# Kernel tuning notes

Measured on AMD Instinct MI355X. Metric: run time of the kernel, lower is better.

## Reference

```python
import jax, jax.numpy as jnp
import numpy as np

N_NODES = 50000


def _gcn_norm(edge_index, num_nodes):
    # PyG GCNConv default: add self-loops, symmetric normalization D^-1/2 A D^-1/2
    src, dst = edge_index[0], edge_index[1]
    loops = jnp.arange(num_nodes, dtype=src.dtype)
    src = jnp.concatenate([src, loops])
    dst = jnp.concatenate([dst, loops])
    deg = jax.ops.segment_sum(jnp.ones_like(src, dtype=jnp.float32), dst,
                              num_segments=num_nodes)
    dis = jnp.where(deg > 0, jax.lax.rsqrt(jnp.maximum(deg, 1.0)), 0.0)
    norm = dis[src] * dis[dst]  # [E']
    return src, dst, norm


def _gcn_conv(x, W, b, src, dst, norm, num_nodes):
    h = x @ W                                   # [N, out] transform first
    msg = h[src] * norm[:, None]                # [E', out] gather + scale
    agg = jax.ops.segment_sum(msg, dst, num_segments=num_nodes)  # scatter-add
    return agg + b


def setup_inputs() -> dict:
    key = jax.random.key(0)
    k1, k2, k3, k4 = jax.random.split(key, 4)
    n, e, d_in, d_h = N_NODES, 800000, 256, 128
    basic_block = jax.random.normal(k1, (n, d_in), dtype=jnp.float32)
    edge_index = jax.random.randint(k2, (2, e), 0, n, dtype=jnp.int64)
    W1 = jax.random.normal(k3, (d_in, d_h), dtype=jnp.float32) * (1.0 / np.sqrt(d_in))
    b1 = jnp.zeros((d_h,), dtype=jnp.float32)
    W2 = jax.random.normal(k4, (d_h, d_h), dtype=jnp.float32) * (1.0 / np.sqrt(d_h))
    b2 = jnp.zeros((d_h,), dtype=jnp.float32)
    return {"basic_block": basic_block, "edge_index": edge_index,
            "W1": W1, "b1": b1, "W2": W2, "b2": b2}


def reference(basic_block, edge_index, W1, b1, W2, b2):
    n = basic_block.shape[0]
    src, dst, norm = _gcn_norm(edge_index, n)
    x = jax.nn.relu(_gcn_conv(basic_block, W1, b1, src, dst, norm, n))
    x = _gcn_conv(x, W2, b2, src, dst, norm, n)
    return x
```

## Files before the change

kernel.cpp:

```cpp
#include <hip/hip_runtime.h>
#include <hip/hip_bf16.h>
#include <stdint.h>

#define D_H 128

typedef __bf16 bf16_t;
typedef unsigned short u16;
typedef bf16_t bf16x8 __attribute__((ext_vector_type(8)));
typedef bf16_t bf16x4 __attribute__((ext_vector_type(4)));
typedef float  f32x4  __attribute__((ext_vector_type(4)));

__global__ void k_countrank(const int* __restrict__ dst, int* __restrict__ cnt,
                            u16* __restrict__ rank, int E) {
    int e = blockIdx.x * 256 + threadIdx.x;
    if (e < E) rank[e] = (u16)atomicAdd(&cnt[dst[e]], 1);
}

__global__ __launch_bounds__(1024) void k_scan1(const int* __restrict__ cnt,
                                                int* __restrict__ out,
                                                int* __restrict__ bsums,
                                                float* __restrict__ dis, int N) {
    __shared__ int tmp[1024];
    int t = threadIdx.x;
    int i = blockIdx.x * 1024 + t;
    int v = (i < N) ? cnt[i] : 0;
    if (i < N) dis[i] = 1.0f / sqrtf((float)(v + 1));
    tmp[t] = v;
    __syncthreads();
    for (int d = 1; d < 1024; d <<= 1) {
        int x = (t >= d) ? tmp[t - d] : 0;
        __syncthreads();
        tmp[t] += x;
        __syncthreads();
    }
    if (i < N) out[i] = tmp[t] - v;
    if (t == 1023) bsums[blockIdx.x] = tmp[t];
}

__global__ void k_scan2(int* __restrict__ bsums, int nb) {
    __shared__ int tmp[64];
    int t = threadIdx.x;
    int v = (t < nb) ? bsums[t] : 0;
    tmp[t] = v;
    __syncthreads();
    for (int d = 1; d < 64; d <<= 1) {
        int x = (t >= d) ? tmp[t - d] : 0;
        __syncthreads();
        tmp[t] += x;
        __syncthreads();
    }
    if (t < nb) bsums[t] = tmp[t] - v;
}

__global__ __launch_bounds__(1024) void k_scan3(int* __restrict__ off,
                                                const int* __restrict__ bsums,
                                                int N, int E) {
    int i = blockIdx.x * 1024 + threadIdx.x;
    if (i < N) off[i] += bsums[blockIdx.x];
    if (i == 0) off[N] = E;
}

__global__ void k_prepw(const float* __restrict__ W, bf16_t* __restrict__ Wh,
                        bf16_t* __restrict__ Wl, int K) {
    int id = blockIdx.x * 256 + threadIdx.x;
    if (id >= K * 128) return;
    int k = id >> 7;
    int n = id & 127;
    float w = W[id];
    bf16_t h = (bf16_t)w;
    bf16_t l = (bf16_t)(w - (float)h);
    Wh[(size_t)n * K + k] = h;
    Wl[(size_t)n * K + k] = l;
}

#define LDK 40
__global__ __launch_bounds__(128) void k_mm1fill(
        const float* __restrict__ Af,
        const bf16_t* __restrict__ Wh, const bf16_t* __restrict__ Wl,
        const float* __restrict__ dis, bf16_t* __restrict__ Cb,
        int N, int K, int mmBlocks,
        const int* __restrict__ src, const int* __restrict__ dst,
        const int* __restrict__ off, const u16* __restrict__ rank,
        u16* __restrict__ csr16, int E) {
    __shared__ bf16_t AsH[64][LDK];
    __shared__ bf16_t AsL[64][LDK];
    __shared__ bf16_t BsH[128][LDK];
    __shared__ bf16_t BsL[128][LDK];

    if ((int)blockIdx.x >= mmBlocks) {
        int e = ((int)blockIdx.x - mmBlocks) * 128 + threadIdx.x;
        if (e < E) {
            int d = dst[e];
            csr16[off[d] + (int)rank[e]] = (u16)src[e];
        }
        return;
    }

    const int t    = threadIdx.x;
    const int lane = t & 63;
    const int wave = t >> 6;
    const int row0 = blockIdx.x * 64;
    const int wn   = wave * 64;
    const int fm   = lane & 15;
    const int fq   = lane >> 4;

    f32x4 acc[4][4] = {};

    for (int k0 = 0; k0 < K; k0 += 32) {
        __syncthreads();
#pragma unroll
        for (int i = 0; i < 4; i++) {
            int idx = t + i * 128;
            int r   = idx >> 3;
            int c4  = idx & 7;
            int gr  = row0 + r;
            float4 v = make_float4(0.f, 0.f, 0.f, 0.f);
            if (gr < N) v = *(const float4*)(Af + (size_t)gr * K + k0 + c4 * 4);
            bf16_t h0 = (bf16_t)v.x, h1 = (bf16_t)v.y, h2 = (bf16_t)v.z, h3 = (bf16_t)v.w;
            bf16_t l0 = (bf16_t)(v.x - (float)h0);
            bf16_t l1 = (bf16_t)(v.y - (float)h1);
            bf16_t l2 = (bf16_t)(v.z - (float)h2);
            bf16_t l3 = (bf16_t)(v.w - (float)h3);
            *(bf16x4*)&AsH[r][c4 * 4] = (bf16x4){h0, h1, h2, h3};
            *(bf16x4*)&AsL[r][c4 * 4] = (bf16x4){l0, l1, l2, l3};
        }
#pragma unroll
        for (int i = 0; i < 4; i++) {
            int idx = t + i * 128;
            int r   = idx >> 2;
            int c8  = idx & 3;
            *(bf16x8*)&BsH[r][c8 * 8] = *(const bf16x8*)(Wh + (size_t)r * K + k0 + c8 * 8);
            *(bf16x8*)&BsL[r][c8 * 8] = *(const bf16x8*)(Wl + (size_t)r * K + k0 + c8 * 8);
        }
        __syncthreads();

        bf16x8 ah[4], al[4], bh[4], bl[4];
#pragma unroll
        for (int i = 0; i < 4; i++) {
            ah[i] = *(const bf16x8*)&AsH[i * 16 + fm][fq * 8];
            al[i] = *(const bf16x8*)&AsL[i * 16 + fm][fq * 8];
            bh[i] = *(const bf16x8*)&BsH[wn + i * 16 + fm][fq * 8];
            bl[i] = *(const bf16x8*)&BsL[wn + i * 16 + fm][fq * 8];
        }
#pragma unroll
        for (int mi = 0; mi < 4; mi++)
#pragma unroll
            for (int ni = 0; ni < 4; ni++) {
                acc[mi][ni] = __builtin_amdgcn_mfma_f32_16x16x32_bf16(ah[mi], bh[ni], acc[mi][ni], 0, 0, 0);
                acc[mi][ni] = __builtin_amdgcn_mfma_f32_16x16x32_bf16(ah[mi], bl[ni], acc[mi][ni], 0, 0, 0);
                acc[mi][ni] = __builtin_amdgcn_mfma_f32_16x16x32_bf16(al[mi], bh[ni], acc[mi][ni], 0, 0, 0);
            }
    }

#pragma unroll
    for (int mi = 0; mi < 4; mi++)
#pragma unroll
        for (int r = 0; r < 4; r++) {
            int grow = row0 + mi * 16 + fq * 4 + r;
            if (grow < N) {
                float dr = dis[grow];
#pragma unroll
                for (int ni = 0; ni < 4; ni++)
                    Cb[(size_t)grow * D_H + wn + ni * 16 + fm] = (bf16_t)(dr * acc[mi][ni][r]);
            }
        }
}

__global__ __launch_bounds__(128) void k_mm2(const bf16_t* __restrict__ Ah,
                                             const bf16_t* __restrict__ Al,
                                             const bf16_t* __restrict__ Wh,
                                             const bf16_t* __restrict__ Wl,
                                             const float* __restrict__ dis,
                                             bf16_t* __restrict__ Cb,
                                             int N, int K) {
    __shared__ bf16_t AsH[64][LDK];
    __shared__ bf16_t AsL[64][LDK];
    __shared__ bf16_t BsH[128][LDK];
    __shared__ bf16_t BsL[128][LDK];

    const int t    = threadIdx.x;
    const int lane = t & 63;
    const int wave = t >> 6;
    const int row0 = blockIdx.x * 64;
    const int wn   = wave * 64;
    const int fm   = lane & 15;
    const int fq   = lane >> 4;

    f32x4 acc[4][4] = {};

    for (int k0 = 0; k0 < K; k0 += 32) {
        __syncthreads();
#pragma unroll
        for (int i = 0; i < 2; i++) {
            int idx = t + i * 128;
            int r   = idx >> 2;
            int c8  = idx & 3;
            int gr  = row0 + r;
            bf16x8 vh = {}, vl = {};
            if (gr < N) {
                vh = *(const bf16x8*)(Ah + (size_t)gr * K + k0 + c8 * 8);
                vl = *(const bf16x8*)(Al + (size_t)gr * K + k0 + c8 * 8);
            }
            *(bf16x8*)&AsH[r][c8 * 8] = vh;
            *(bf16x8*)&AsL[r][c8 * 8] = vl;
        }
#pragma unroll
        for (int i = 0; i < 4; i++) {
            int idx = t + i * 128;
            int r   = idx >> 2;
            int c8  = idx & 3;
            *(bf16x8*)&BsH[r][c8 * 8] = *(const bf16x8*)(Wh + (size_t)r * K + k0 + c8 * 8);
            *(bf16x8*)&BsL[r][c8 * 8] = *(const bf16x8*)(Wl + (size_t)r * K + k0 + c8 * 8);
        }
        __syncthreads();

        bf16x8 ah[4], al[4], bh[4], bl[4];
#pragma unroll
        for (int i = 0; i < 4; i++) {
            ah[i] = *(const bf16x8*)&AsH[i * 16 + fm][fq * 8];
            al[i] = *(const bf16x8*)&AsL[i * 16 + fm][fq * 8];
            bh[i] = *(const bf16x8*)&BsH[wn + i * 16 + fm][fq * 8];
            bl[i] = *(const bf16x8*)&BsL[wn + i * 16 + fm][fq * 8];
        }
#pragma unroll
        for (int mi = 0; mi < 4; mi++)
#pragma unroll
            for (int ni = 0; ni < 4; ni++) {
                acc[mi][ni] = __builtin_amdgcn_mfma_f32_16x16x32_bf16(ah[mi], bh[ni], acc[mi][ni], 0, 0, 0);
                acc[mi][ni] = __builtin_amdgcn_mfma_f32_16x16x32_bf16(ah[mi], bl[ni], acc[mi][ni], 0, 0, 0);
                acc[mi][ni] = __builtin_amdgcn_mfma_f32_16x16x32_bf16(al[mi], bh[ni], acc[mi][ni], 0, 0, 0);
            }
    }

#pragma unroll
    for (int mi = 0; mi < 4; mi++)
#pragma unroll
        for (int r = 0; r < 4; r++) {
            int grow = row0 + mi * 16 + fq * 4 + r;
            if (grow < N) {
                float dr = dis[grow];
#pragma unroll
                for (int ni = 0; ni < 4; ni++)
                    Cb[(size_t)grow * D_H + wn + ni * 16 + fm] = (bf16_t)(dr * acc[mi][ni][r]);
            }
        }
}

__global__ __launch_bounds__(256) void k_agg(const bf16_t* __restrict__ Hb,
                                             const float* __restrict__ dis,
                                             const int* __restrict__ off,
                                             const u16* __restrict__ csr16,
                                             const float4* __restrict__ bias4,
                                             float4* __restrict__ outF,
                                             bf16_t* __restrict__ outH,
                                             bf16_t* __restrict__ outL,
                                             int N, int mode) {
    const int half = threadIdx.x >> 5;
    const int lane = threadIdx.x & 31;
    const int node = blockIdx.x * 8 + half;
    if (node >= N) return;

    const size_t loff = (size_t)lane * 4;

    bf16x4 vs = *(const bf16x4*)(Hb + (size_t)node * D_H + loff);
    float4 a0 = make_float4((float)vs[0], (float)vs[1], (float)vs[2], (float)vs[3]);
    float4 a1 = {0,0,0,0}, a2 = {0,0,0,0}, a3 = {0,0,0,0};
    float4 a4 = {0,0,0,0}, a5 = {0,0,0,0}, a6 = {0,0,0,0}, a7 = {0,0,0,0};

    int p  = off[node];
    int p1 = off[node + 1];

    for (; p + 8 <= p1; p += 8) {
        int s0 = (int)csr16[p + 0], s1 = (int)csr16[p + 1];
        int s2 = (int)csr16[p + 2], s3 = (int)csr16[p + 3];
        int s4 = (int)csr16[p + 4], s5 = (int)csr16[p + 5];
        int s6 = (int)csr16[p + 6], s7 = (int)csr16[p + 7];
        bf16x4 h0 = *(const bf16x4*)(Hb + (size_t)s0 * D_H + loff);
        bf16x4 h1 = *(const bf16x4*)(Hb + (size_t)s1 * D_H + loff);
        bf16x4 h2 = *(const bf16x4*)(Hb + (size_t)s2 * D_H + loff);
        bf16x4 h3 = *(const bf16x4*)(Hb + (size_t)s3 * D_H + loff);
        bf16x4 h4 = *(const bf16x4*)(Hb + (size_t)s4 * D_H + loff);
        bf16x4 h5 = *(const bf16x4*)(Hb + (size_t)s5 * D_H + loff);
        bf16x4 h6 = *(const bf16x4*)(Hb + (size_t)s6 * D_H + loff);
        bf16x4 h7 = *(const bf16x4*)(Hb + (size_t)s7 * D_H + loff);
        a0.x += (float)h0[0]; a0.y += (float)h0[1]; a0.z += (float)h0[2]; a0.w += (float)h0[3];
        a1.x += (float)h1[0]; a1.y += (float)h1[1]; a1.z += (float)h1[2]; a1.w += (float)h1[3];
        a2.x += (float)h2[0]; a2.y += (float)h2[1]; a2.z += (float)h2[2]; a2.w += (float)h2[3];
        a3.x += (float)h3[0]; a3.y += (float)h3[1]; a3.z += (float)h3[2]; a3.w += (float)h3[3];
        a4.x += (float)h4[0]; a4.y += (float)h4[1]; a4.z += (float)h4[2]; a4.w += (float)h4[3];
        a5.x += (float)h5[0]; a5.y += (float)h5[1]; a5.z += (float)h5[2]; a5.w += (float)h5[3];
        a6.x += (float)h6[0]; a6.y += (float)h6[1]; a6.z += (float)h6[2]; a6.w += (float)h6[3];
        a7.x += (float)h7[0]; a7.y += (float)h7[1]; a7.z += (float)h7[2]; a7.w += (float)h7[3];
    }
    if (p + 4 <= p1) {
        int s0 = (int)csr16[p + 0], s1 = (int)csr16[p + 1];
        int s2 = (int)csr16[p + 2], s3 = (int)csr16[p + 3];
        bf16x4 h0 = *(const bf16x4*)(Hb + (size_t)s0 * D_H + loff);
        bf16x4 h1 = *(const bf16x4*)(Hb + (size_t)s1 * D_H + loff);
        bf16x4 h2 = *(const bf16x4*)(Hb + (size_t)s2 * D_H + loff);
        bf16x4 h3 = *(const bf16x4*)(Hb + (size_t)s3 * D_H + loff);
        a0.x += (float)h0[0]; a0.y += (float)h0[1]; a0.z += (float)h0[2]; a0.w += (float)h0[3];
        a1.x += (float)h1[0]; a1.y += (float)h1[1]; a1.z += (float)h1[2]; a1.w += (float)h1[3];
        a2.x += (float)h2[0]; a2.y += (float)h2[1]; a2.z += (float)h2[2]; a2.w += (float)h2[3];
        a3.x += (float)h3[0]; a3.y += (float)h3[1]; a3.z += (float)h3[2]; a3.w += (float)h3[3];
        p += 4;
    }
    for (; p < p1; p++) {
        int s0 = (int)csr16[p];
        bf16x4 h0 = *(const bf16x4*)(Hb + (size_t)s0 * D_H + loff);
        a0.x += (float)h0[0]; a0.y += (float)h0[1]; a0.z += (float)h0[2]; a0.w += (float)h0[3];
    }

    float4 sum;
    sum.x = ((a0.x + a1.x) + (a2.x + a3.x)) + ((a4.x + a5.x) + (a6.x + a7.x));
    sum.y = ((a0.y + a1.y) + (a2.y + a3.y)) + ((a4.y + a5.y) + (a6.y + a7.y));
    sum.z = ((a0.z + a1.z) + (a2.z + a3.z)) + ((a4.z + a5.z) + (a6.z + a7.z));
    sum.w = ((a0.w + a1.w) + (a2.w + a3.w)) + ((a4.w + a5.w) + (a6.w + a7.w));

    const float  di = dis[node];
    const float4 bv = bias4[lane];
    float vx = fmaf(di, sum.x, bv.x);
    float vy = fmaf(di, sum.y, bv.y);
    float vz = fmaf(di, sum.z, bv.z);
    float vw = fmaf(di, sum.w, bv.w);

    if (mode == 1) {
        vx = fmaxf(vx, 0.0f); vy = fmaxf(vy, 0.0f);
        vz = fmaxf(vz, 0.0f); vw = fmaxf(vw, 0.0f);
        bf16_t hx = (bf16_t)vx, hy = (bf16_t)vy, hz = (bf16_t)vz, hw = (bf16_t)vw;
        bf16_t lx = (bf16_t)(vx - (float)hx);
        bf16_t ly = (bf16_t)(vy - (float)hy);
        bf16_t lz = (bf16_t)(vz - (float)hz);
        bf16_t lw = (bf16_t)(vw - (float)hw);
        *(bf16x4*)(outH + (size_t)node * D_H + loff) = (bf16x4){hx, hy, hz, hw};
        *(bf16x4*)(outL + (size_t)node * D_H + loff) = (bf16x4){lx, ly, lz, lw};
    } else {
        outF[(size_t)node * 32 + lane] = make_float4(vx, vy, vz, vw);
    }
}

extern "C" void kernel_launch(void* const* d_in, const int* in_sizes, int n_in,
                              void* d_out, int out_size, void* d_ws, size_t ws_size,
                              hipStream_t stream) {
    const float* X  = (const float*)d_in[0];
    const int*   ei = (const int*)d_in[1];
    const float* W1 = (const float*)d_in[2];
    const float* b1 = (const float*)d_in[3];
    const float* W2 = (const float*)d_in[4];
    const float* b2 = (const float*)d_in[5];
    float* out = (float*)d_out;

    const int N  = in_sizes[0] / 256;
    const int E  = in_sizes[1] / 2;
    const int K1 = 256;

    const int* src = ei;
    const int* dst = ei + E;

    uintptr_t p = (uintptr_t)d_ws;
    auto carve = [&](size_t bytes) {
        uintptr_t q = p;
        p += (bytes + 255) & ~(size_t)255;
        return q;
    };
    int*    cnt   = (int*)carve((size_t)N * 4);
    int*    off   = (int*)carve((size_t)(N + 1) * 4);
    int*    bsums = (int*)carve(64 * 4);
    float*  dis   = (float*)carve((size_t)N * 4);
    u16*    rank  = (u16*)carve((size_t)E * 2);
    u16*    csr16 = (u16*)carve((size_t)E * 2);
    bf16_t* Hb    = (bf16_t*)carve((size_t)N * D_H * 2);
    bf16_t* X1h   = (bf16_t*)carve((size_t)N * D_H * 2);
    bf16_t* X1l   = (bf16_t*)carve((size_t)N * D_H * 2);
    bf16_t* W1h   = (bf16_t*)carve((size_t)K1 * D_H * 2);
    bf16_t* W1l   = (bf16_t*)carve((size_t)K1 * D_H * 2);
    bf16_t* W2h   = (bf16_t*)carve((size_t)D_H * D_H * 2);
    bf16_t* W2l   = (bf16_t*)carve((size_t)D_H * D_H * 2);

    const int nb = (N + 1023) / 1024;

    k_prepw<<<(K1 * 128 + 255) / 256, 256, 0, stream>>>(W1, W1h, W1l, K1);
    k_prepw<<<(D_H * 128 + 255) / 256, 256, 0, stream>>>(W2, W2h, W2l, D_H);

    hipMemsetAsync(cnt, 0, (size_t)N * 4, stream);
    k_countrank<<<(E + 255) / 256, 256, 0, stream>>>(dst, cnt, rank, E);
    k_scan1<<<nb, 1024, 0, stream>>>(cnt, off, bsums, dis, N);
    k_scan2<<<1, 64, 0, stream>>>(bsums, nb);
    k_scan3<<<nb, 1024, 0, stream>>>(off, bsums, N, E);

    const int gmm  = (N + 63) / 64;
    const int gfil = (E + 127) / 128;
    const int gag  = (N + 7) / 8;

    k_mm1fill<<<gmm + gfil, 128, 0, stream>>>(X, W1h, W1l, dis, Hb, N, K1, gmm,
                                              src, dst, off, rank, csr16, E);
    k_agg<<<gag, 256, 0, stream>>>(Hb, dis, off, csr16,
                                   (const float4*)b1, nullptr, X1h, X1l, N, 1);

    k_mm2<<<gmm, 128, 0, stream>>>(X1h, X1l, W2h, W2l, dis, Hb, N, D_H);
    k_agg<<<gag, 256, 0, stream>>>(Hb, dis, off, csr16,
                                   (const float4*)b2, (float4*)out, nullptr, nullptr, N, 0);
}
```

Before: 271.0 us.

## Fold weight prep into count kernel and spread CSR fill across GEMM blocks

```diff
diff --git a/kernel.cpp b/kernel.cpp
--- a/kernel.cpp
+++ b/kernel.cpp
@@ -11,9 +11,32 @@
 typedef float  f32x4  __attribute__((ext_vector_type(4)));
 
 __global__ void k_countrank(const int* __restrict__ dst, int* __restrict__ cnt,
-                            u16* __restrict__ rank, int E) {
-    int e = blockIdx.x * 256 + threadIdx.x;
-    if (e < E) rank[e] = (u16)atomicAdd(&cnt[dst[e]], 1);
+                            u16* __restrict__ rank, int E, int crBlocks,
+                            const float* __restrict__ W1, bf16_t* __restrict__ W1h,
+                            bf16_t* __restrict__ W1l, int K1,
+                            const float* __restrict__ W2, bf16_t* __restrict__ W2h,
+                            bf16_t* __restrict__ W2l, int K2) {
+    if ((int)blockIdx.x < crBlocks) {
+        int e = blockIdx.x * 256 + threadIdx.x;
+        if (e < E) rank[e] = (u16)atomicAdd(&cnt[dst[e]], 1);
+        return;
+    }
+    int id = ((int)blockIdx.x - crBlocks) * 256 + threadIdx.x;
+    int n1 = K1 * 128;
+    if (id < n1) {
+        int k = id >> 7, n = id & 127;
+        float w = W1[id];
+        bf16_t h = (bf16_t)w;
+        W1h[(size_t)n * K1 + k] = h;
+        W1l[(size_t)n * K1 + k] = (bf16_t)(w - (float)h);
+    } else if (id < n1 + K2 * 128) {
+        int id2 = id - n1;
+        int k = id2 >> 7, n = id2 & 127;
+        float w = W2[id2];
+        bf16_t h = (bf16_t)w;
+        W2h[(size_t)n * K2 + k] = h;
+        W2l[(size_t)n * K2 + k] = (bf16_t)(w - (float)h);
+    }
 }
 
 __global__ __launch_bounds__(1024) void k_scan1(const int* __restrict__ cnt,
@@ -60,41 +83,20 @@
     if (i == 0) off[N] = E;
 }
 
-__global__ void k_prepw(const float* __restrict__ W, bf16_t* __restrict__ Wh,
-                        bf16_t* __restrict__ Wl, int K) {
-    int id = blockIdx.x * 256 + threadIdx.x;
-    if (id >= K * 128) return;
-    int k = id >> 7;
-    int n = id & 127;
-    float w = W[id];
-    bf16_t h = (bf16_t)w;
-    bf16_t l = (bf16_t)(w - (float)h);
-    Wh[(size_t)n * K + k] = h;
-    Wl[(size_t)n * K + k] = l;
-}
-
 #define LDK 40
+#define FILL_PER 8
 __global__ __launch_bounds__(128) void k_mm1fill(
         const float* __restrict__ Af,
         const bf16_t* __restrict__ Wh, const bf16_t* __restrict__ Wl,
         const float* __restrict__ dis, bf16_t* __restrict__ Cb,
-        int N, int K, int mmBlocks,
+        int N, int K,
         const int* __restrict__ src, const int* __restrict__ dst,
         const int* __restrict__ off, const u16* __restrict__ rank,
-        u16* __restrict__ csr16, int E) {
+        u16* __restrict__ csr16, int E, int totThreads) {
     __shared__ bf16_t AsH[64][LDK];
     __shared__ bf16_t AsL[64][LDK];
     __shared__ bf16_t BsH[128][LDK];
     __shared__ bf16_t BsL[128][LDK];
-
-    if ((int)blockIdx.x >= mmBlocks) {
-        int e = ((int)blockIdx.x - mmBlocks) * 128 + threadIdx.x;
-        if (e < E) {
-            int d = dst[e];
-            csr16[off[d] + (int)rank[e]] = (u16)src[e];
-        }
-        return;
-    }
 
     const int t    = threadIdx.x;
     const int lane = t & 63;
@@ -103,6 +105,22 @@
     const int wn   = wave * 64;
     const int fm   = lane & 15;
     const int fq   = lane >> 4;
+
+    const int g = blockIdx.x * 128 + t;
+    int epos[FILL_PER];
+    u16 esrc[FILL_PER];
+#pragma unroll
+    for (int i = 0; i < FILL_PER; i++) {
+        int e = g + i * totThreads;
+        if (e < E) {
+            int d = dst[e];
+            epos[i] = off[d] + (int)rank[e];
+            esrc[i] = (u16)src[e];
+        } else {
+            epos[i] = -1;
+            esrc[i] = 0;
+        }
+    }
 
     f32x4 acc[4][4] = {};
 
@@ -164,6 +182,10 @@
                     Cb[(size_t)grow * D_H + wn + ni * 16 + fm] = (bf16_t)(dr * acc[mi][ni][r]);
             }
         }
+
+#pragma unroll
+    for (int i = 0; i < FILL_PER; i++)
+        if (epos[i] >= 0) csr16[epos[i]] = esrc[i];
 }
 
 __global__ __launch_bounds__(128) void k_mm2(const bf16_t* __restrict__ Ah,
@@ -379,21 +401,21 @@
 
     const int nb = (N + 1023) / 1024;
 
-    k_prepw<<<(K1 * 128 + 255) / 256, 256, 0, stream>>>(W1, W1h, W1l, K1);
-    k_prepw<<<(D_H * 128 + 255) / 256, 256, 0, stream>>>(W2, W2h, W2l, D_H);
-
     hipMemsetAsync(cnt, 0, (size_t)N * 4, stream);
-    k_countrank<<<(E + 255) / 256, 256, 0, stream>>>(dst, cnt, rank, E);
+    const int gcr   = (E + 255) / 256;
+    const int gprep = (K1 * 128 + D_H * 128 + 255) / 256;
+    k_countrank<<<gcr + gprep, 256, 0, stream>>>(dst, cnt, rank, E, gcr,
+                                                 W1, W1h, W1l, K1,
+                                                 W2, W2h, W2l, D_H);
     k_scan1<<<nb, 1024, 0, stream>>>(cnt, off, bsums, dis, N);
     k_scan2<<<1, 64, 0, stream>>>(bsums, nb);
     k_scan3<<<nb, 1024, 0, stream>>>(off, bsums, N, E);
 
-    const int gmm  = (N + 63) / 64;
-    const int gfil = (E + 127) / 128;
-    const int gag  = (N + 7) / 8;
-
-    k_mm1fill<<<gmm + gfil, 128, 0, stream>>>(X, W1h, W1l, dis, Hb, N, K1, gmm,
-                                              src, dst, off, rank, csr16, E);
+    const int gmm = (N + 63) / 64;
+    const int gag = (N + 7) / 8;
+
+    k_mm1fill<<<gmm, 128, 0, stream>>>(X, W1h, W1l, dis, Hb, N, K1,
+                                       src, dst, off, rank, csr16, E, gmm * 128);
     k_agg<<<gag, 256, 0, stream>>>(Hb, dis, off, csr16,
                                    (const float4*)b1, nullptr, X1h, X1l, N, 1);
 
```

Result: faster. 265.4 us (-2.1%).
